# Performance work log

Measured on AMD Instinct MI355X. Metric: run time of the kernel, lower is better.

## Reference

```python
import jax, jax.numpy as jnp
import numpy as np

B, N, Q, D = 1, 6, 10000, 256
HEADS, LEVELS, NPTS, ZANCH = 8, 1, 8, 4  # NPTS = 2*n_points, ZANCH = num_points_in_pillar
HF, WF = 32, 88
HD = D // HEADS


def setup_inputs() -> dict:
    key = jax.random.key(0)
    ks = jax.random.split(key, 18)
    s = 1.0 / np.sqrt(D)
    inp = {
        'queries': jax.random.normal(ks[0], (B, N, Q, D), jnp.float32),
        'pos_emb': jax.random.normal(ks[1], (B, N, Q, D), jnp.float32),
        'lvl_emb': jax.random.normal(ks[2], (LEVELS, D), jnp.float32),
        'cam_emb': jax.random.normal(ks[3], (N, D), jnp.float32),
        'features0': jax.random.normal(ks[4], (B * N, D, HF, WF), jnp.float32),
        'reference_points_3D': jax.random.uniform(ks[5], (B, N, Q, ZANCH, 2), jnp.float32),
        'bev_mask': jax.random.randint(ks[6], (B, N, Q, ZANCH, 2), 0, 2).astype(bool),
        # MSDeformAttn3D params
        'W_value': jax.random.normal(ks[7], (D, D), jnp.float32) * s,
        'b_value': jnp.zeros((D,), jnp.float32),
        'W_off': jax.random.normal(ks[8], (HEADS * LEVELS * NPTS * 2, D), jnp.float32) * 0.01,
        'b_off': jax.random.uniform(ks[9], (HEADS * LEVELS * NPTS * 2,), jnp.float32, -2.0, 2.0),
        'W_attn': jax.random.normal(ks[10], (HEADS * LEVELS * NPTS, D), jnp.float32) * s,
        'b_attn': jnp.zeros((HEADS * LEVELS * NPTS,), jnp.float32),
        'W_inner': jax.random.normal(ks[11], (D, D), jnp.float32) * s,
        'b_inner': jnp.zeros((D,), jnp.float32),
        # SpatialCrossAttention.output_proj
        'W_out': jax.random.normal(ks[12], (D, D), jnp.float32) * s,
        'b_out': jnp.zeros((D,), jnp.float32),
    }
    return inp


def _bilinear(value_t, loc, H, W):
    # value_t: (bn, heads, H*W, hd); loc: (bn, q, heads, pts, 2) normalized to [0,1]
    bn, q, heads, pts, _ = loc.shape
    hd = value_t.shape[-1]
    # grid_sample(2*loc-1, align_corners=False) -> pixel coord = loc*size - 0.5
    x = loc[..., 0] * W - 0.5
    y = loc[..., 1] * H - 0.5
    x0 = jnp.floor(x); y0 = jnp.floor(y)
    dx = x - x0; dy = y - y0
    x0 = x0.astype(jnp.int32); y0 = y0.astype(jnp.int32)
    out = jnp.zeros((bn, heads, q * pts, hd), value_t.dtype)
    corners = ((0, 0, (1 - dx) * (1 - dy)), (1, 0, dx * (1 - dy)),
               (0, 1, (1 - dx) * dy), (1, 1, dx * dy))
    for ox, oy, w in corners:
        xi = x0 + ox; yi = y0 + oy
        valid = (xi >= 0) & (xi < W) & (yi >= 0) & (yi < H)  # zero padding
        wgt = jnp.where(valid, w, 0.0)
        idx = jnp.clip(yi, 0, H - 1) * W + jnp.clip(xi, 0, W - 1)  # (bn,q,heads,pts)
        idx_t = idx.transpose(0, 2, 1, 3).reshape(bn, heads, q * pts)
        g = jnp.take_along_axis(value_t, idx_t[..., None], axis=2)  # (bn,heads,q*pts,hd)
        wgt_t = wgt.transpose(0, 2, 1, 3).reshape(bn, heads, q * pts)
        out = out + g * wgt_t[..., None]
    return out.reshape(bn, heads, q, pts, hd)


def _forward(queries, pos_emb, lvl_emb, cam_emb, features0, reference_points_3D, bev_mask,
             W_value, b_value, W_off, b_off, W_attn, b_attn, W_inner, b_inner, W_out, b_out):
    b, n, q, d = queries.shape
    hf, wf = features0.shape[-2:]
    # flatten features + level/cam embeddings -> (b*n, hw, d)
    feat = features0.reshape(b, n, d, hf * wf)
    feat = feat + lvl_emb[0][None, None, :, None] + cam_emb[None, :, :, None]
    input_flatten = feat.transpose(0, 1, 3, 2).reshape(b * n, hf * wf, d)

    qp = (queries + pos_emb).reshape(b * n, q, d)
    ref = reference_points_3D.reshape(b * n, q, ZANCH, 2)

    # --- MSDeformAttn3D (single level) ---
    value = (input_flatten @ W_value.T + b_value).reshape(b * n, hf * wf, HEADS, HD)
    off = (qp @ W_off.T + b_off).reshape(b * n, q, HEADS, LEVELS, NPTS, 2)
    attw = jax.nn.softmax((qp @ W_attn.T + b_attn).reshape(b * n, q, HEADS, LEVELS * NPTS), axis=-1)
    attw = attw.reshape(b * n, q, HEADS, LEVELS, NPTS)
    normalizer = jnp.array([wf, hf], queries.dtype)  # (W, H)
    pts_per_z = NPTS // ZANCH
    off_z = off.reshape(b * n, q, HEADS, LEVELS, pts_per_z, ZANCH, 2)
    loc = ref[:, :, None, None, None, :, :] + off_z / normalizer
    loc = loc.reshape(b * n, q, HEADS, LEVELS, NPTS, 2)

    value_t = value.transpose(0, 2, 1, 3)  # (bn, heads, hw, hd)
    sampled = _bilinear(value_t, loc[:, :, :, 0], hf, wf)  # (bn,heads,q,pts,hd)
    attw_t = attw[:, :, :, 0].transpose(0, 2, 1, 3)  # (bn,heads,q,pts)
    out = jnp.einsum('bhqp,bhqpc->bqhc', attw_t, sampled).reshape(b * n, q, d)
    out = out @ W_inner.T + b_inner

    # --- scatter back per camera, normalize by hit count ---
    attn = out.reshape(b, n, q, d)
    # indexes come from batch 0's mask (as in the original code)
    hit = (bev_mask[0, :, :, :, 0].astype(jnp.int32).sum(-1) > 0).astype(queries.dtype)  # (n,q)
    slots = (attn * hit[None, :, :, None]).sum(1)  # (b,q,d)
    count = (bev_mask[..., 0].astype(jnp.int32).sum(-1) > 0).astype(queries.dtype).sum(1)
    count = jnp.clip(count, 1.0, None)  # (b,q)
    slots = slots / count[..., None]
    return slots @ W_out.T + b_out


def reference(queries, pos_emb, lvl_emb, cam_emb, features0, reference_points_3D, bev_mask,
              W_value, b_value, W_off, b_off, W_attn, b_attn, W_inner, b_inner, W_out, b_out):
    return _forward(queries, pos_emb, lvl_emb, cam_emb, features0, reference_points_3D, bev_mask,
                    W_value, b_value, W_off, b_off, W_attn, b_attn, W_inner, b_inner, W_out, b_out)
```

## Files before the change

### kernel.cpp

```cpp
#include <hip/hip_runtime.h>
#include <hip/hip_bf16.h>

#define BN     6
#define NQ     10000
#define DIM    256
#define HEADS  8
#define HDD    32
#define HF_    32
#define WF_    88
#define HW_    (HF_*WF_)
#define MTOT   (BN*NQ)

typedef __attribute__((ext_vector_type(8))) unsigned short ushort8_t;
typedef __attribute__((ext_vector_type(8))) short bf16x8;
typedef __attribute__((ext_vector_type(4))) float f32x4;

static __device__ inline unsigned short f2bf(float x) {
    __hip_bfloat16 b = __float2bfloat16(x);
    return *(unsigned short*)&b;
}

__global__ __launch_bounds__(256)
void k_wcvt(const float* __restrict__ Wv, const float* __restrict__ Wo,
            const float* __restrict__ Wa, const float* __restrict__ Wi,
            const float* __restrict__ Wz,
            unsigned short* __restrict__ Wv_bf, unsigned short* __restrict__ Woa_bf,
            unsigned short* __restrict__ Wi_bf, unsigned short* __restrict__ Wz_bf)
{
    const int i4 = (blockIdx.x*256 + threadIdx.x) * 4;
    if (i4 < 65536) {
        float4 v;
        ushort4 p;
        v = *(const float4*)(Wv+i4); p.x=f2bf(v.x);p.y=f2bf(v.y);p.z=f2bf(v.z);p.w=f2bf(v.w);
        *(ushort4*)(Wv_bf+i4) = p;
        v = *(const float4*)(Wi+i4); p.x=f2bf(v.x);p.y=f2bf(v.y);p.z=f2bf(v.z);p.w=f2bf(v.w);
        *(ushort4*)(Wi_bf+i4) = p;
        v = *(const float4*)(Wz+i4); p.x=f2bf(v.x);p.y=f2bf(v.y);p.z=f2bf(v.z);p.w=f2bf(v.w);
        *(ushort4*)(Wz_bf+i4) = p;
    }
    if (i4 < 32768) {
        float4 v = *(const float4*)(Wo+i4);
        ushort4 p; p.x=f2bf(v.x);p.y=f2bf(v.y);p.z=f2bf(v.z);p.w=f2bf(v.w);
        *(ushort4*)(Woa_bf+i4) = p;
    }
    if (i4 < 16384) {
        float4 v = *(const float4*)(Wa+i4);
        ushort4 p; p.x=f2bf(v.x);p.y=f2bf(v.y);p.z=f2bf(v.z);p.w=f2bf(v.w);
        *(ushort4*)(Woa_bf+32768+i4) = p;
    }
}

__global__ __launch_bounds__(256)
void k_ebias(const float* __restrict__ lvl, const float* __restrict__ cam,
             const float* __restrict__ Wv, const float* __restrict__ bv,
             float* __restrict__ ebias)
{
    const int n = blockIdx.x;
    const int j = threadIdx.x;
    __shared__ float e[DIM];
    e[j] = lvl[j] + cam[n*DIM + j];
    __syncthreads();
    const float* w = Wv + (size_t)j*DIM;
    float s = bv[j];
    for (int d = 0; d < DIM; ++d) s += e[d]*w[d];
    ebias[n*DIM + j] = s;
}

__global__ __launch_bounds__(256)
void k_mask(const int* __restrict__ bev, float* __restrict__ hitf,
            float* __restrict__ scale, float* __restrict__ biasf)
{
    const int q = blockIdx.x*256 + threadIdx.x;
    if (q >= NQ) return;
    float cnt = 0.f;
    #pragma unroll
    for (int n = 0; n < BN; ++n) {
        int hit = 0;
        #pragma unroll
        for (int z = 0; z < 4; ++z)
            hit |= (bev[(((size_t)n*NQ + q)*4 + z)*2] != 0);
        hitf[(size_t)n*NQ + q] = (float)hit;
        cnt += (float)hit;
    }
    biasf[q] = (cnt > 0.f) ? 1.f : 0.f;
    scale[q] = 1.f / fmaxf(cnt, 1.f);
}

__global__ __launch_bounds__(256)
void k_feat(const float* __restrict__ feat, unsigned short* __restrict__ featT)
{
    __shared__ float Tf[64][68];
    const int cam = blockIdx.z;
    const int d0 = blockIdx.y * 64;
    const int p0 = blockIdx.x * 64;
    const int tid = threadIdx.x;
    #pragma unroll
    for (int i = 0; i < 4; ++i) {
        const int d = (tid>>4) + i*16;
        const int p4 = (tid&15)*4;
        *(float4*)&Tf[d][p4] = *(const float4*)(feat + ((size_t)cam*DIM + d0 + d)*HW_ + p0 + p4);
    }
    __syncthreads();
    const int p = tid>>2, dq = tid&3;
    unsigned short* ob = featT + ((size_t)cam*HW_ + p0 + p)*DIM + d0;
    #pragma unroll
    for (int i = 0; i < 4; ++i) {
        const int d4 = dq*4 + i*16;
        ushort4 pk;
        pk.x = f2bf(Tf[d4+0][p]); pk.y = f2bf(Tf[d4+1][p]);
        pk.z = f2bf(Tf[d4+2][p]); pk.w = f2bf(Tf[d4+3][p]);
        *(ushort4*)(ob + d4) = pk;
    }
}

__global__ __launch_bounds__(256)
void k_value_mfma(const unsigned short* __restrict__ featT,
                  const unsigned short* __restrict__ Wv_bf,
                  const float* __restrict__ ebias,
                  unsigned short* __restrict__ value_bf)
{
    __shared__ unsigned short Ap[128][72];
    __shared__ unsigned short Bc[64][72];
    const int cam = blockIdx.z;
    const int p0 = blockIdx.x * 128;
    const int c0 = blockIdx.y * 64;
    const int tid = threadIdx.x;
    const int lane = tid & 63, wave = tid >> 6;
    const int quad = lane >> 4, l15 = lane & 15;
    f32x4 acc[2][4] = {};
    const unsigned short* fbase = featT + ((size_t)cam*HW_ + p0)*DIM;

    for (int k0 = 0; k0 < DIM; k0 += 64) {
        #pragma unroll
        for (int i = 0; i < 4; ++i) {
            const int row = (tid>>3) + i*32;
            const int k8 = (tid&7)*8;
            *(ushort8_t*)&Ap[row][k8] = *(const ushort8_t*)(fbase + (size_t)row*DIM + k0 + k8);
        }
        #pragma unroll
        for (int i = 0; i < 2; ++i) {
            const int row = (tid>>3) + i*32;
            const int k8 = (tid&7)*8;
            *(ushort8_t*)&Bc[row][k8] = *(const ushort8_t*)(Wv_bf + (size_t)(c0+row)*DIM + k0 + k8);
        }
        __syncthreads();
        #pragma unroll
        for (int s = 0; s < 2; ++s) {
            const int kf = s*32 + quad*8;
            bf16x8 a[2], b[4];
            #pragma unroll
            for (int mt = 0; mt < 2; ++mt)
                a[mt] = *(const bf16x8*)&Ap[(wave*2+mt)*16 + l15][kf];
            #pragma unroll
            for (int nt = 0; nt < 4; ++nt)
                b[nt] = *(const bf16x8*)&Bc[nt*16 + l15][kf];
            #pragma unroll
            for (int mt = 0; mt < 2; ++mt)
                #pragma unroll
                for (int nt = 0; nt < 4; ++nt)
                    acc[mt][nt] = __builtin_amdgcn_mfma_f32_16x16x32_bf16(a[mt], b[nt], acc[mt][nt], 0,0,0);
        }
        __syncthreads();
    }
    #pragma unroll
    for (int nt = 0; nt < 4; ++nt) {
        const int c = c0 + nt*16 + l15;
        const float eb = ebias[cam*DIM + c];
        const int h = c >> 5, cc = c & 31;
        unsigned short* vb = value_bf + (size_t)(cam*HEADS + h)*HW_*HDD + cc;
        #pragma unroll
        for (int mt = 0; mt < 2; ++mt)
            #pragma unroll
            for (int r = 0; r < 4; ++r) {
                const int p = p0 + (wave*2+mt)*16 + quad*4 + r;
                vb[(size_t)p*HDD] = f2bf(acc[mt][nt][r] + eb);
            }
    }
}

__global__ __launch_bounds__(256, 3)
void k_offattn(const float* __restrict__ Qr, const float* __restrict__ Pe,
               const unsigned short* __restrict__ Woa_bf,
               const float* __restrict__ boff, const float* __restrict__ battn,
               float* __restrict__ off_ws, float* __restrict__ attw_ws)
{
    __shared__ char smraw[32*204*4];
    unsigned short (*A_lds)[264] = (unsigned short (*)[264])smraw;
    float (*C_lds)[204] = (float (*)[204])smraw;

    const int m0 = blockIdx.x * 32;
    const int tid = threadIdx.x;
    const int lane = tid & 63, wave = tid >> 6;
    const int quad = lane >> 4, l15 = lane & 15;
    const int n0 = wave * 48;

    bf16x8 breg[3][8];
    #pragma unroll
    for (int nt = 0; nt < 3; ++nt) {
        const unsigned short* wb = Woa_bf + (size_t)(n0 + nt*16 + l15)*DIM + quad*8;
        #pragma unroll
        for (int kc = 0; kc < 8; ++kc)
            breg[nt][kc] = *(const bf16x8*)(wb + kc*32);
    }

    {
        const int row = tid >> 3;
        const int c8  = tid & 7;
        const float* qb = Qr + (size_t)(m0 + row)*DIM;
        const float* pb = Pe + (size_t)(m0 + row)*DIM;
        #pragma unroll
        for (int j = 0; j < 8; ++j) {
            const int col = c8*4 + j*32;
            const float4 x = *(const float4*)(qb + col);
            const float4 y = *(const float4*)(pb + col);
            ushort4 pk;
            pk.x = f2bf(x.x+y.x); pk.y = f2bf(x.y+y.y);
            pk.z = f2bf(x.z+y.z); pk.w = f2bf(x.w+y.w);
            *(ushort4*)&A_lds[row][col] = pk;
        }
    }
    __syncthreads();

    f32x4 acc[2][3] = {};
    #pragma unroll
    for (int kc = 0; kc < 8; ++kc) {
        const int kk = kc*32 + quad*8;
        const bf16x8 a0 = *(const bf16x8*)&A_lds[l15][kk];
        const bf16x8 a1 = *(const bf16x8*)&A_lds[16 + l15][kk];
        #pragma unroll
        for (int nt = 0; nt < 3; ++nt) {
            acc[0][nt] = __builtin_amdgcn_mfma_f32_16x16x32_bf16(a0, breg[nt][kc], acc[0][nt], 0,0,0);
            acc[1][nt] = __builtin_amdgcn_mfma_f32_16x16x32_bf16(a1, breg[nt][kc], acc[1][nt], 0,0,0);
        }
    }

    __syncthreads();
    #pragma unroll
    for (int nt = 0; nt < 3; ++nt) {
        const int col = n0 + nt*16 + l15;
        const float bias = (col < 128) ? boff[col] : battn[col-128];
        #pragma unroll
        for (int mt = 0; mt < 2; ++mt) {
            #pragma unroll
            for (int r = 0; r < 4; ++r)
                C_lds[mt*16 + quad*4 + r][col] = acc[mt][nt][r] + bias;
        }
    }
    __syncthreads();
    {
        float* a = &C_lds[tid>>3][128 + (tid&7)*8];
        float lg[8];
        float mx = -1e30f;
        #pragma unroll
        for (int p = 0; p < 8; ++p) { lg[p] = a[p]; mx = fmaxf(mx, lg[p]); }
        float ssum = 0.f;
        #pragma unroll
        for (int p = 0; p < 8; ++p) { lg[p] = __expf(lg[p]-mx); ssum += lg[p]; }
        const float inv = 1.f/ssum;
        #pragma unroll
        for (int p = 0; p < 8; ++p) a[p] = lg[p]*inv;
    }
    __syncthreads();
    #pragma unroll
    for (int i = 0; i < 4; ++i) {
        const int idx = i*256 + tid;
        const int row = idx >> 5, c4 = (idx & 31)*4;
        *(float4*)(off_ws + ((size_t)(m0+row))*128 + c4) = *(float4*)&C_lds[row][c4];
    }
    #pragma unroll
    for (int i = 0; i < 2; ++i) {
        const int idx = i*256 + tid;
        const int row = idx >> 4, c4 = (idx & 15)*4;
        *(float4*)(attw_ws + ((size_t)(m0+row))*64 + c4) = *(float4*)&C_lds[row][128 + c4];
    }
}

__global__ __launch_bounds__(256)
void k_sample(const unsigned short* __restrict__ value_bf,
              const float* __restrict__ off_ws, const float* __restrict__ attw_ws,
              const float* __restrict__ ref3d, const float* __restrict__ hitf,
              const float* __restrict__ scale, unsigned short* __restrict__ asum_bf)
{
    const int q0 = blockIdx.x * 8;
    const int tid = threadIdx.x;

    __shared__ float s_off[8][128];
    __shared__ float s_att[8][64];
    __shared__ float s_ref[8][8];
    __shared__ float s_hit[BN][8];
    __shared__ float s_scl[8];

    if (tid < 48) s_hit[tid>>3][tid&7] = hitf[(size_t)(tid>>3)*NQ + q0 + (tid&7)];
    if (tid < 8)  s_scl[tid] = scale[q0 + tid];

    const int quarter = tid & 3;
    const int h  = (tid >> 2) & 7;
    const int ql = tid >> 5;

    float acc[8];
    #pragma unroll
    for (int c = 0; c < 8; ++c) acc[c] = 0.f;

    for (int n = 0; n < BN; ++n) {
        __syncthreads();
        {
            const float4* so = (const float4*)(off_ws + ((size_t)n*NQ + q0)*128);
            ((float4*)&s_off[0][0])[tid] = so[tid];
            const float2* sa = (const float2*)(attw_ws + ((size_t)n*NQ + q0)*64);
            ((float2*)&s_att[0][0])[tid] = sa[tid];
            if (tid < 64)
                (&s_ref[0][0])[tid] = (ref3d + ((size_t)n*NQ + q0)*8)[tid];
        }
        __syncthreads();

        if (s_hit[n][ql] != 0.f) {
            const unsigned short* vbase =
                value_bf + (size_t)(n*HEADS + h)*HW_*HDD + quarter*8;

            #pragma unroll
            for (int p = 0; p < 8; ++p) {
                const int z = p & 3;
                const float wp = s_att[ql][h*8+p];
                const float ax = s_ref[ql][z*2+0]*WF_ + s_off[ql][h*16+p*2+0] - 0.5f;
                const float ay = s_ref[ql][z*2+1]*HF_ + s_off[ql][h*16+p*2+1] - 0.5f;
                const float fx = floorf(ax), fy = floorf(ay);
                const float dx = ax-fx, dy = ay-fy;
                const int x0 = (int)fx, y0 = (int)fy;
                #pragma unroll
                for (int oy = 0; oy < 2; ++oy) {
                    const int yi = y0 + oy;
                    const float wy = oy ? dy : 1.f-dy;
                    #pragma unroll
                    for (int ox = 0; ox < 2; ++ox) {
                        const int xi = x0 + ox;
                        const float wx = ox ? dx : 1.f-dx;
                        const bool valid = ((unsigned)xi < WF_) & ((unsigned)yi < HF_);
                        const float cw = valid ? wp*wy*wx : 0.f;
                        const int xc = min(max(xi, 0), WF_-1);
                        const int yc = min(max(yi, 0), HF_-1);
                        const ushort8_t v = *(const ushort8_t*)(vbase + (size_t)(yc*WF_ + xc)*HDD);
                        #pragma unroll
                        for (int c = 0; c < 8; ++c)
                            acc[c] += cw * __uint_as_float(((unsigned)v[c]) << 16);
                    }
                }
            }
        }
    }

    const float sc = s_scl[ql];
    ushort8_t o;
    #pragma unroll
    for (int c = 0; c < 8; ++c) o[c] = f2bf(acc[c]*sc);
    *(ushort8_t*)(asum_bf + ((size_t)(q0+ql))*DIM + h*HDD + quarter*8) = o;
}

__global__ __launch_bounds__(256)
void k_gemm_mfma(const unsigned short* __restrict__ A_bf,
                 const unsigned short* __restrict__ W_bf,
                 const float* __restrict__ bias, const float* __restrict__ rowscale,
                 float* __restrict__ out_f, unsigned short* __restrict__ out_b, int M)
{
    __shared__ unsigned short As[128][72];
    __shared__ unsigned short Bs[64][72];
    const int m0 = blockIdx.x * 128;
    const int j0 = blockIdx.y * 64;
    const int tid = threadIdx.x;
    const int lane = tid & 63, wave = tid >> 6;
    const int quad = lane >> 4, l15 = lane & 15;
    f32x4 acc[2][4] = {};

    for (int k0 = 0; k0 < DIM; k0 += 64) {
        #pragma unroll
        for (int i = 0; i < 4; ++i) {
            const int row = (tid>>3) + i*32;
            const int k8 = (tid&7)*8;
            ushort8_t v = {0,0,0,0,0,0,0,0};
            if (m0 + row < M)
                v = *(const ushort8_t*)(A_bf + (size_t)(m0+row)*DIM + k0 + k8);
            *(ushort8_t*)&As[row][k8] = v;
        }
        #pragma unroll
        for (int i = 0; i < 2; ++i) {
            const int row = (tid>>3) + i*32;
            const int k8 = (tid&7)*8;
            *(ushort8_t*)&Bs[row][k8] = *(const ushort8_t*)(W_bf + (size_t)(j0+row)*DIM + k0 + k8);
        }
        __syncthreads();
        #pragma unroll
        for (int s = 0; s < 2; ++s) {
            const int kf = s*32 + quad*8;
            bf16x8 a[2], b[4];
            #pragma unroll
            for (int mt = 0; mt < 2; ++mt)
                a[mt] = *(const bf16x8*)&As[(wave*2+mt)*16 + l15][kf];
            #pragma unroll
            for (int nt = 0; nt < 4; ++nt)
                b[nt] = *(const bf16x8*)&Bs[nt*16 + l15][kf];
            #pragma unroll
            for (int mt = 0; mt < 2; ++mt)
                #pragma unroll
                for (int nt = 0; nt < 4; ++nt)
                    acc[mt][nt] = __builtin_amdgcn_mfma_f32_16x16x32_bf16(a[mt], b[nt], acc[mt][nt], 0,0,0);
        }
        __syncthreads();
    }
    #pragma unroll
    for (int nt = 0; nt < 4; ++nt) {
        const int j = j0 + nt*16 + l15;
        const float bj = bias[j];
        #pragma unroll
        for (int mt = 0; mt < 2; ++mt) {
            #pragma unroll
            for (int r = 0; r < 4; ++r) {
                const int m = m0 + (wave*2+mt)*16 + quad*4 + r;
                if (m >= M) continue;
                const float f = rowscale ? rowscale[m] : 1.f;
                const float v = acc[mt][nt][r] + f*bj;
                if (out_f) out_f[(size_t)m*DIM + j] = v;
                if (out_b) out_b[(size_t)m*DIM + j] = f2bf(v);
            }
        }
    }
}

extern "C" void kernel_launch(void* const* d_in, const int* in_sizes, int n_in,
                              void* d_out, int out_size, void* d_ws, size_t ws_size,
                              hipStream_t stream)
{
    const float* queries = (const float*)d_in[0];
    const float* pos_emb = (const float*)d_in[1];
    const float* lvl_emb = (const float*)d_in[2];
    const float* cam_emb = (const float*)d_in[3];
    const float* features= (const float*)d_in[4];
    const float* ref3d   = (const float*)d_in[5];
    const int*   bev     = (const int*)d_in[6];
    const float* Wv = (const float*)d_in[7];
    const float* bv = (const float*)d_in[8];
    const float* Wo = (const float*)d_in[9];
    const float* bo = (const float*)d_in[10];
    const float* Wa = (const float*)d_in[11];
    const float* ba = (const float*)d_in[12];
    const float* Wi = (const float*)d_in[13];
    const float* bi = (const float*)d_in[14];
    const float* Wz = (const float*)d_in[15];
    const float* bz = (const float*)d_in[16];
    float* out = (float*)d_out;

    char* ws = (char*)d_ws;
    size_t o = 0;
    auto alloc = [&](size_t bytes) { char* p = ws + o; o += (bytes + 255) & ~size_t(255); return p; };
    unsigned short* value_bf = (unsigned short*)alloc((size_t)BN*HEADS*HW_*HDD*2);
    unsigned short* featT    = (unsigned short*)alloc((size_t)BN*HW_*DIM*2);
    float* off_ws   = (float*)alloc((size_t)MTOT*128*4);
    float* attw_ws  = (float*)alloc((size_t)MTOT*64*4);
    unsigned short* asum_bf  = (unsigned short*)alloc((size_t)NQ*DIM*2);
    unsigned short* slots_bf = (unsigned short*)alloc((size_t)NQ*DIM*2);
    unsigned short* Wv_bf  = (unsigned short*)alloc(65536*2);
    unsigned short* Woa_bf = (unsigned short*)alloc(49152*2);
    unsigned short* Wi_bf  = (unsigned short*)alloc(65536*2);
    unsigned short* Wz_bf  = (unsigned short*)alloc(65536*2);
    float* hitf   = (float*)alloc((size_t)BN*NQ*4);
    float* scalev = (float*)alloc(NQ*4);
    float* biasf  = (float*)alloc(NQ*4);
    float* ebias  = (float*)alloc(BN*DIM*4);

    k_wcvt  <<<64, 256, 0, stream>>>(Wv, Wo, Wa, Wi, Wz, Wv_bf, Woa_bf, Wi_bf, Wz_bf);
    k_ebias <<<BN, 256, 0, stream>>>(lvl_emb, cam_emb, Wv, bv, ebias);
    k_mask  <<<(NQ+255)/256, 256, 0, stream>>>(bev, hitf, scalev, biasf);
    k_feat  <<<dim3(HW_/64, DIM/64, BN), 256, 0, stream>>>(features, featT);
    k_value_mfma<<<dim3(HW_/128, DIM/64, BN), 256, 0, stream>>>(featT, Wv_bf, ebias, value_bf);
    k_offattn<<<MTOT/32, 256, 0, stream>>>(queries, pos_emb, Woa_bf, bo, ba, off_ws, attw_ws);
    k_sample <<<NQ/8, 256, 0, stream>>>(value_bf, off_ws, attw_ws, ref3d, hitf, scalev, asum_bf);
    k_gemm_mfma<<<dim3((NQ+127)/128, DIM/64), 256, 0, stream>>>(asum_bf, Wi_bf, bi, biasf, nullptr, slots_bf, NQ);
    k_gemm_mfma<<<dim3((NQ+127)/128, DIM/64), 256, 0, stream>>>(slots_bf, Wz_bf, bz, nullptr, out, nullptr, NQ);
}
```

Baseline: 342.6 us.

## Fuse prep kernels into one launch and chain inner/output GEMMs per tile

Merges the weight conversion, embedding-bias and mask kernels into a single launch that dispatches on block index. Replaces the two back-to-back GEMMs (inner projection, then output projection) with one kernel. Each block computes 32 rows of the first GEMM, keeps the bf16 intermediate in LDS, runs the second GEMM from there, and stages results through LDS for coalesced float4 stores. This removes two launches and the intermediate global round trip. In exchange, B operands are read straight from global memory without LDS tiling, and each block covers all 256 columns.

```diff
diff --git a/kernel.cpp b/kernel.cpp
--- a/kernel.cpp
+++ b/kernel.cpp
@@ -21,69 +21,66 @@
 }
 
 __global__ __launch_bounds__(256)
-void k_wcvt(const float* __restrict__ Wv, const float* __restrict__ Wo,
+void k_prep(const float* __restrict__ Wv, const float* __restrict__ Wo,
             const float* __restrict__ Wa, const float* __restrict__ Wi,
             const float* __restrict__ Wz,
+            const float* __restrict__ lvl, const float* __restrict__ cam,
+            const float* __restrict__ bv, const int* __restrict__ bev,
             unsigned short* __restrict__ Wv_bf, unsigned short* __restrict__ Woa_bf,
-            unsigned short* __restrict__ Wi_bf, unsigned short* __restrict__ Wz_bf)
-{
-    const int i4 = (blockIdx.x*256 + threadIdx.x) * 4;
-    if (i4 < 65536) {
-        float4 v;
-        ushort4 p;
-        v = *(const float4*)(Wv+i4); p.x=f2bf(v.x);p.y=f2bf(v.y);p.z=f2bf(v.z);p.w=f2bf(v.w);
-        *(ushort4*)(Wv_bf+i4) = p;
-        v = *(const float4*)(Wi+i4); p.x=f2bf(v.x);p.y=f2bf(v.y);p.z=f2bf(v.z);p.w=f2bf(v.w);
-        *(ushort4*)(Wi_bf+i4) = p;
-        v = *(const float4*)(Wz+i4); p.x=f2bf(v.x);p.y=f2bf(v.y);p.z=f2bf(v.z);p.w=f2bf(v.w);
-        *(ushort4*)(Wz_bf+i4) = p;
-    }
-    if (i4 < 32768) {
-        float4 v = *(const float4*)(Wo+i4);
-        ushort4 p; p.x=f2bf(v.x);p.y=f2bf(v.y);p.z=f2bf(v.z);p.w=f2bf(v.w);
-        *(ushort4*)(Woa_bf+i4) = p;
-    }
-    if (i4 < 16384) {
-        float4 v = *(const float4*)(Wa+i4);
-        ushort4 p; p.x=f2bf(v.x);p.y=f2bf(v.y);p.z=f2bf(v.z);p.w=f2bf(v.w);
-        *(ushort4*)(Woa_bf+32768+i4) = p;
-    }
-}
-
-__global__ __launch_bounds__(256)
-void k_ebias(const float* __restrict__ lvl, const float* __restrict__ cam,
-             const float* __restrict__ Wv, const float* __restrict__ bv,
-             float* __restrict__ ebias)
-{
-    const int n = blockIdx.x;
-    const int j = threadIdx.x;
-    __shared__ float e[DIM];
-    e[j] = lvl[j] + cam[n*DIM + j];
-    __syncthreads();
-    const float* w = Wv + (size_t)j*DIM;
-    float s = bv[j];
-    for (int d = 0; d < DIM; ++d) s += e[d]*w[d];
-    ebias[n*DIM + j] = s;
-}
-
-__global__ __launch_bounds__(256)
-void k_mask(const int* __restrict__ bev, float* __restrict__ hitf,
+            unsigned short* __restrict__ Wi_bf, unsigned short* __restrict__ Wz_bf,
+            float* __restrict__ ebias, float* __restrict__ hitf,
             float* __restrict__ scale, float* __restrict__ biasf)
 {
-    const int q = blockIdx.x*256 + threadIdx.x;
-    if (q >= NQ) return;
-    float cnt = 0.f;
-    #pragma unroll
-    for (int n = 0; n < BN; ++n) {
-        int hit = 0;
-        #pragma unroll
-        for (int z = 0; z < 4; ++z)
-            hit |= (bev[(((size_t)n*NQ + q)*4 + z)*2] != 0);
-        hitf[(size_t)n*NQ + q] = (float)hit;
-        cnt += (float)hit;
-    }
-    biasf[q] = (cnt > 0.f) ? 1.f : 0.f;
-    scale[q] = 1.f / fmaxf(cnt, 1.f);
+    const int b = blockIdx.x;
+    const int tid = threadIdx.x;
+    if (b < 64) {
+        const int i4 = (b*256 + tid) * 4;
+        if (i4 < 65536) {
+            float4 v;
+            ushort4 p;
+            v = *(const float4*)(Wv+i4); p.x=f2bf(v.x);p.y=f2bf(v.y);p.z=f2bf(v.z);p.w=f2bf(v.w);
+            *(ushort4*)(Wv_bf+i4) = p;
+            v = *(const float4*)(Wi+i4); p.x=f2bf(v.x);p.y=f2bf(v.y);p.z=f2bf(v.z);p.w=f2bf(v.w);
+            *(ushort4*)(Wi_bf+i4) = p;
+            v = *(const float4*)(Wz+i4); p.x=f2bf(v.x);p.y=f2bf(v.y);p.z=f2bf(v.z);p.w=f2bf(v.w);
+            *(ushort4*)(Wz_bf+i4) = p;
+        }
+        if (i4 < 32768) {
+            float4 v = *(const float4*)(Wo+i4);
+            ushort4 p; p.x=f2bf(v.x);p.y=f2bf(v.y);p.z=f2bf(v.z);p.w=f2bf(v.w);
+            *(ushort4*)(Woa_bf+i4) = p;
+        }
+        if (i4 < 16384) {
+            float4 v = *(const float4*)(Wa+i4);
+            ushort4 p; p.x=f2bf(v.x);p.y=f2bf(v.y);p.z=f2bf(v.z);p.w=f2bf(v.w);
+            *(ushort4*)(Woa_bf+32768+i4) = p;
+        }
+    } else if (b < 70) {
+        const int n = b - 64;
+        const int j = tid;
+        __shared__ float e[DIM];
+        e[j] = lvl[j] + cam[n*DIM + j];
+        __syncthreads();
+        const float* w = Wv + (size_t)j*DIM;
+        float s = bv[j];
+        for (int d = 0; d < DIM; ++d) s += e[d]*w[d];
+        ebias[n*DIM + j] = s;
+    } else {
+        const int q = (b - 70)*256 + tid;
+        if (q >= NQ) return;
+        float cnt = 0.f;
+        #pragma unroll
+        for (int n = 0; n < BN; ++n) {
+            int hit = 0;
+            #pragma unroll
+            for (int z = 0; z < 4; ++z)
+                hit |= (bev[(((size_t)n*NQ + q)*4 + z)*2] != 0);
+            hitf[(size_t)n*NQ + q] = (float)hit;
+            cnt += (float)hit;
+        }
+        biasf[q] = (cnt > 0.f) ? 1.f : 0.f;
+        scale[q] = 1.f / fmaxf(cnt, 1.f);
+    }
 }
 
 __global__ __launch_bounds__(256)
@@ -356,71 +353,89 @@
 }
 
 __global__ __launch_bounds__(256)
-void k_gemm_mfma(const unsigned short* __restrict__ A_bf,
-                 const unsigned short* __restrict__ W_bf,
-                 const float* __restrict__ bias, const float* __restrict__ rowscale,
-                 float* __restrict__ out_f, unsigned short* __restrict__ out_b, int M)
-{
-    __shared__ unsigned short As[128][72];
-    __shared__ unsigned short Bs[64][72];
-    const int m0 = blockIdx.x * 128;
-    const int j0 = blockIdx.y * 64;
+void k_tail(const unsigned short* __restrict__ asum_bf,
+            const unsigned short* __restrict__ Wi_bf,
+            const unsigned short* __restrict__ Wz_bf,
+            const float* __restrict__ bi, const float* __restrict__ bz,
+            const float* __restrict__ biasf, float* __restrict__ out)
+{
+    __shared__ char smraw[32*260*4];
+    unsigned short (*S_lds)[264] = (unsigned short (*)[264])smraw;
+    float (*C_lds)[260] = (float (*)[260])smraw;
+
+    const int m0 = blockIdx.x * 32;
     const int tid = threadIdx.x;
     const int lane = tid & 63, wave = tid >> 6;
     const int quad = lane >> 4, l15 = lane & 15;
+    const int n0 = wave * 64;
+
+    const int r0 = m0 + l15;
+    const int r1 = m0 + 16 + l15;
+    const unsigned short* a0p = asum_bf + (size_t)(r0 < NQ ? r0 : 0)*DIM;
+    const unsigned short* a1p = asum_bf + (size_t)(r1 < NQ ? r1 : 0)*DIM;
+
     f32x4 acc[2][4] = {};
-
-    for (int k0 = 0; k0 < DIM; k0 += 64) {
-        #pragma unroll
-        for (int i = 0; i < 4; ++i) {
-            const int row = (tid>>3) + i*32;
-            const int k8 = (tid&7)*8;
-            ushort8_t v = {0,0,0,0,0,0,0,0};
-            if (m0 + row < M)
-                v = *(const ushort8_t*)(A_bf + (size_t)(m0+row)*DIM + k0 + k8);
-            *(ushort8_t*)&As[row][k8] = v;
-        }
-        #pragma unroll
-        for (int i = 0; i < 2; ++i) {
-            const int row = (tid>>3) + i*32;
-            const int k8 = (tid&7)*8;
-            *(ushort8_t*)&Bs[row][k8] = *(const ushort8_t*)(W_bf + (size_t)(j0+row)*DIM + k0 + k8);
-        }
-        __syncthreads();
-        #pragma unroll
-        for (int s = 0; s < 2; ++s) {
-            const int kf = s*32 + quad*8;
-            bf16x8 a[2], b[4];
-            #pragma unroll
-            for (int mt = 0; mt < 2; ++mt)
-                a[mt] = *(const bf16x8*)&As[(wave*2+mt)*16 + l15][kf];
-            #pragma unroll
-            for (int nt = 0; nt < 4; ++nt)
-                b[nt] = *(const bf16x8*)&Bs[nt*16 + l15][kf];
-            #pragma unroll
-            for (int mt = 0; mt < 2; ++mt)
-                #pragma unroll
-                for (int nt = 0; nt < 4; ++nt)
-                    acc[mt][nt] = __builtin_amdgcn_mfma_f32_16x16x32_bf16(a[mt], b[nt], acc[mt][nt], 0,0,0);
-        }
-        __syncthreads();
+    #pragma unroll
+    for (int kc = 0; kc < 8; ++kc) {
+        const int kk = kc*32 + quad*8;
+        const bf16x8 a0 = *(const bf16x8*)(a0p + kk);
+        const bf16x8 a1 = *(const bf16x8*)(a1p + kk);
+        #pragma unroll
+        for (int nt = 0; nt < 4; ++nt) {
+            const bf16x8 b = *(const bf16x8*)(Wi_bf + (size_t)(n0 + nt*16 + l15)*DIM + kk);
+            acc[0][nt] = __builtin_amdgcn_mfma_f32_16x16x32_bf16(a0, b, acc[0][nt], 0,0,0);
+            acc[1][nt] = __builtin_amdgcn_mfma_f32_16x16x32_bf16(a1, b, acc[1][nt], 0,0,0);
+        }
     }
     #pragma unroll
     for (int nt = 0; nt < 4; ++nt) {
-        const int j = j0 + nt*16 + l15;
-        const float bj = bias[j];
+        const int col = n0 + nt*16 + l15;
+        const float bj = bi[col];
         #pragma unroll
         for (int mt = 0; mt < 2; ++mt) {
             #pragma unroll
             for (int r = 0; r < 4; ++r) {
-                const int m = m0 + (wave*2+mt)*16 + quad*4 + r;
-                if (m >= M) continue;
-                const float f = rowscale ? rowscale[m] : 1.f;
-                const float v = acc[mt][nt][r] + f*bj;
-                if (out_f) out_f[(size_t)m*DIM + j] = v;
-                if (out_b) out_b[(size_t)m*DIM + j] = f2bf(v);
+                const int m = m0 + mt*16 + quad*4 + r;
+                const float f = (m < NQ) ? biasf[m] : 0.f;
+                S_lds[mt*16 + quad*4 + r][col] = f2bf(acc[mt][nt][r] + f*bj);
             }
         }
+    }
+    __syncthreads();
+
+    f32x4 acc2[2][4] = {};
+    #pragma unroll
+    for (int kc = 0; kc < 8; ++kc) {
+        const int kk = kc*32 + quad*8;
+        const bf16x8 s0 = *(const bf16x8*)&S_lds[l15][kk];
+        const bf16x8 s1 = *(const bf16x8*)&S_lds[16 + l15][kk];
+        #pragma unroll
+        for (int nt = 0; nt < 4; ++nt) {
+            const bf16x8 b = *(const bf16x8*)(Wz_bf + (size_t)(n0 + nt*16 + l15)*DIM + kk);
+            acc2[0][nt] = __builtin_amdgcn_mfma_f32_16x16x32_bf16(s0, b, acc2[0][nt], 0,0,0);
+            acc2[1][nt] = __builtin_amdgcn_mfma_f32_16x16x32_bf16(s1, b, acc2[1][nt], 0,0,0);
+        }
+    }
+    __syncthreads();
+    #pragma unroll
+    for (int nt = 0; nt < 4; ++nt) {
+        const int col = n0 + nt*16 + l15;
+        const float bj = bz[col];
+        #pragma unroll
+        for (int mt = 0; mt < 2; ++mt) {
+            #pragma unroll
+            for (int r = 0; r < 4; ++r)
+                C_lds[mt*16 + quad*4 + r][col] = acc2[mt][nt][r] + bj;
+        }
+    }
+    __syncthreads();
+    #pragma unroll
+    for (int i = 0; i < 8; ++i) {
+        const int idx = i*256 + tid;
+        const int row = idx >> 6, c4 = (idx & 63)*4;
+        const int m = m0 + row;
+        if (m < NQ)
+            *(float4*)(out + (size_t)m*DIM + c4) = *(float4*)&C_lds[row][c4];
     }
 }
 
@@ -455,7 +470,6 @@
     float* off_ws   = (float*)alloc((size_t)MTOT*128*4);
     float* attw_ws  = (float*)alloc((size_t)MTOT*64*4);
     unsigned short* asum_bf  = (unsigned short*)alloc((size_t)NQ*DIM*2);
-    unsigned short* slots_bf = (unsigned short*)alloc((size_t)NQ*DIM*2);
     unsigned short* Wv_bf  = (unsigned short*)alloc(65536*2);
     unsigned short* Woa_bf = (unsigned short*)alloc(49152*2);
     unsigned short* Wi_bf  = (unsigned short*)alloc(65536*2);
@@ -465,13 +479,12 @@
     float* biasf  = (float*)alloc(NQ*4);
     float* ebias  = (float*)alloc(BN*DIM*4);
 
-    k_wcvt  <<<64, 256, 0, stream>>>(Wv, Wo, Wa, Wi, Wz, Wv_bf, Woa_bf, Wi_bf, Wz_bf);
-    k_ebias <<<BN, 256, 0, stream>>>(lvl_emb, cam_emb, Wv, bv, ebias);
-    k_mask  <<<(NQ+255)/256, 256, 0, stream>>>(bev, hitf, scalev, biasf);
+    k_prep  <<<110, 256, 0, stream>>>(Wv, Wo, Wa, Wi, Wz, lvl_emb, cam_emb, bv, bev,
+                                      Wv_bf, Woa_bf, Wi_bf, Wz_bf,
+                                      ebias, hitf, scalev, biasf);
     k_feat  <<<dim3(HW_/64, DIM/64, BN), 256, 0, stream>>>(features, featT);
     k_value_mfma<<<dim3(HW_/128, DIM/64, BN), 256, 0, stream>>>(featT, Wv_bf, ebias, value_bf);
     k_offattn<<<MTOT/32, 256, 0, stream>>>(queries, pos_emb, Woa_bf, bo, ba, off_ws, attw_ws);
     k_sample <<<NQ/8, 256, 0, stream>>>(value_bf, off_ws, attw_ws, ref3d, hitf, scalev, asum_bf);
-    k_gemm_mfma<<<dim3((NQ+127)/128, DIM/64), 256, 0, stream>>>(asum_bf, Wi_bf, bi, biasf, nullptr, slots_bf, NQ);
-    k_gemm_mfma<<<dim3((NQ+127)/128, DIM/64), 256, 0, stream>>>(slots_bf, Wz_bf, bz, nullptr, out, nullptr, NQ);
-}
+    k_tail   <<<(NQ+31)/32, 256, 0, stream>>>(asum_bf, Wi_bf, Wz_bf, bi, bz, biasf, out);
+}
```

New measurement: 325.8 us. 1.05x faster.
